# Optimization experiments

Hardware: AMD Instinct MI355X
Metric: run time of the kernel (lower is better)

## Reference

```python
import jax, jax.numpy as jnp
import numpy as np

S, N, B, EMB = 20, 102400, 1024, 64


def setup_inputs() -> dict:
    key = jax.random.key(0)
    ks = jax.random.split(key, 8)
    nodes_abs = jax.random.normal(ks[0], (S, N, 2), jnp.float32) * 5.0
    nodes_norm = jax.random.normal(ks[1], (S, N, 2), jnp.float32)
    shift_value = jax.random.normal(ks[2], (S, N, 2), jnp.float32)
    seq_list = jax.random.uniform(ks[3], (S, N), jnp.float32) - 0.02
    scenes = jnp.arange(B, dtype=jnp.int32)
    pednum = jnp.full((B,), N // B, dtype=jnp.int32)  # peds per scene
    # TSModel stand-in parameters (2 -> EMB -> 2 with GM-history mixing)
    W_in = jax.random.normal(ks[4], (2, EMB), jnp.float32) * 0.5
    W_gm = jax.random.normal(ks[5], (EMB, EMB), jnp.float32) * (1.0 / np.sqrt(EMB))
    b_h = jnp.zeros((EMB,), jnp.float32)
    W_out = jax.random.normal(ks[6], (EMB, 2), jnp.float32) * (1.0 / np.sqrt(EMB))
    b_out = jnp.zeros((2,), jnp.float32)
    return {"nodes_abs": nodes_abs, "nodes_norm": nodes_norm, "shift_value": shift_value,
            "seq_list": seq_list, "scenes": scenes, "pednum": pednum,
            "W_in": W_in, "W_gm": W_gm, "b_h": b_h, "W_out": W_out, "b_out": b_out}


def reference(nodes_abs, nodes_norm, shift_value, seq_list, scenes, pednum,
              W_in, W_gm, b_h, W_out, b_out):
    S_, N_, _ = nodes_abs.shape
    B_ = pednum.shape[0]
    # scene id per pedestrian from cumsum(pednum) -- replaces get_st_ed slices
    scene_ids = jnp.searchsorted(jnp.cumsum(pednum), jnp.arange(N_), side="right")
    presence = seq_list > 0

    def step(carry, xs):
        mask, gm_sum = carry            # mask: [N] peds present in all frames 0..f
        pres_f, abs_f, f = xs
        mask = mask & pres_f            # get_node_index(seq_list[:f+1])
        mf = mask.astype(abs_f.dtype)   # [N]
        # center_alignment_spa: per-scene mean over active peds at frame f
        cnt = jax.ops.segment_sum(mf, scene_ids, num_segments=B_)
        ssum = jax.ops.segment_sum(abs_f * mf[:, None], scene_ids, num_segments=B_)
        center = ssum / jnp.maximum(cnt, 1.0)[:, None]            # [B,2]
        coord = (abs_f - center[scene_ids]) * mf[:, None]         # [N,2]
        # TSModel stand-in: embed centered coord + running GM-history mean
        gm_mean = gm_sum / jnp.maximum(f, 1).astype(gm_sum.dtype)  # mean of GM[:f]
        h = jnp.tanh(coord @ W_in + gm_mean @ W_gm + b_h) * mf[:, None]  # [N,EMB]
        out = (h @ W_out + b_out) * mf[:, None]                    # masked scatter write
        return (mask, gm_sum + h), out

    mask0 = jnp.ones((N_,), dtype=bool)
    gm0 = jnp.zeros((N_, W_gm.shape[0]), nodes_abs.dtype)
    xs = (presence[: S_ - 1], nodes_abs[: S_ - 1], jnp.arange(S_ - 1))
    _, outs = jax.lax.scan(step, (mask0, gm0), xs)                # [S-1,N,2]
    outputs = jnp.concatenate([outs, jnp.zeros((1, N_, 2), outs.dtype)], axis=0)
    return outputs
```

## Files before the change

### kernel.cpp

```cpp
#include <hip/hip_runtime.h>

#define S_DIM 20
#define NSTEP 19
#define EMB   64
#define GSTR  72
#define MAXP  128

typedef __attribute__((ext_vector_type(8))) short bf16x8;
typedef __attribute__((ext_vector_type(4))) float f32x4;

__device__ __forceinline__ uint32_t pk_bf16(float lo, float hi) {
    uint32_t r;
    asm("v_cvt_pk_bf16_f32 %0, %1, %2" : "=v"(r) : "v"(lo), "v"(hi));
    return r;
}
__device__ __forceinline__ short bf16s(float v) { return (short)(pk_bf16(v, v) & 0xffffu); }
__device__ __forceinline__ float unbf16(uint32_t lo16) {
    union { uint32_t u; float f; } c; c.u = lo16 << 16; return c.f;
}

__global__ __launch_bounds__(256, 4) void pfa_kernel(
    const float* __restrict__ nodes_abs,
    const float* __restrict__ seq_list,
    const int*   __restrict__ pednum,
    const float* __restrict__ W_in,
    const float* __restrict__ W_gm,
    const float* __restrict__ b_h,
    const float* __restrict__ W_out,
    const float* __restrict__ b_out,
    float*       __restrict__ out,
    int N, int B)
{
    const int b    = blockIdx.x;
    const int t    = threadIdx.x;
    const int lane = t & 63;
    const int w    = t >> 6;
    const int l15  = lane & 15;
    const int hi   = lane >> 4;

    __shared__ __attribute__((aligned(16))) uint32_t G[8 * 16 * GSTR];
    __shared__ uint32_t masks[MAXP];
    __shared__ float2   cxy[NSTEP];

    int partial = 0;
    for (int i = lane; i < b; i += 64) partial += pednum[i];
    #pragma unroll
    for (int off = 32; off; off >>= 1) partial += __shfl_xor(partial, off, 64);
    const int start = partial;
    const int P = min(pednum[b], MAXP);
    const int q = (P + 7) >> 3;

    {
        uint4* g4 = (uint4*)&G[(w * 2) * 16 * GSTR];
        for (int i = lane; i < 2 * 16 * GSTR / 4; i += 64)
            g4[i] = make_uint4(0u, 0u, 0u, 0u);
    }

    bf16x8 agm[4][2];
    #pragma unroll
    for (int m = 0; m < 4; ++m)
        #pragma unroll
        for (int T = 0; T < 2; ++T)
            #pragma unroll
            for (int e = 0; e < 8; ++e)
                agm[m][T][e] = bf16s(W_gm[(32*T + 8*hi + e) * EMB + 16*m + l15]);

    bf16x8 aaug[4];
    #pragma unroll
    for (int m = 0; m < 4; ++m) {
        bf16x8 a = {0,0,0,0,0,0,0,0};
        if (hi == 0) {
            const int j = 16*m + l15;
            const float w0 = W_in[j], w1 = W_in[EMB + j], bh = b_h[j];
            const short w0h = bf16s(w0); const short w0l = bf16s(w0 - unbf16((uint16_t)w0h));
            const short w1h = bf16s(w1); const short w1l = bf16s(w1 - unbf16((uint16_t)w1h));
            const short bhh = bf16s(bh); const short bhl = bf16s(bh - unbf16((uint16_t)bhh));
            a[0]=w0h; a[1]=w0l; a[2]=w0h; a[3]=w1h; a[4]=w1l; a[5]=w1h; a[6]=bhh; a[7]=bhl;
        }
        aaug[m] = a;
    }

    bf16x8 aout[2];
    #pragma unroll
    for (int T = 0; T < 2; ++T)
        #pragma unroll
        for (int e = 0; e < 8; ++e) {
            const int j = 32*T + 8*hi + e;
            aout[T][e] = (l15 < 2) ? bf16s(W_out[j*2 + l15]) : (short)0;
        }
    const float bo0 = b_out[0], bo1 = b_out[1];

    if (t < P) {
        uint32_t m = 0; bool alive = true;
        #pragma unroll
        for (int f = 0; f < NSTEP; ++f) {
            alive = alive && (seq_list[(size_t)f * N + start + t] > 0.0f);
            m |= (alive ? 1u : 0u) << f;
        }
        masks[t] = m;
    }
    __syncthreads();

    for (int f = w; f < NSTEP; f += 4) {
        float cnt = 0.f, sx = 0.f, sy = 0.f;
        for (int p = lane; p < P; p += 64) {
            const float mf = (float)((masks[p] >> f) & 1u);
            const float2 a = *(const float2*)&nodes_abs[((size_t)f * N + start + p) * 2];
            cnt += mf; sx = fmaf(a.x, mf, sx); sy = fmaf(a.y, mf, sy);
        }
        #pragma unroll
        for (int off = 32; off; off >>= 1) {
            cnt += __shfl_xor(cnt, off, 64);
            sx  += __shfl_xor(sx , off, 64);
            sy  += __shfl_xor(sy , off, 64);
        }
        if (lane == 0) {
            const float ic = __builtin_amdgcn_rcpf(fmaxf(cnt, 1.0f));
            cxy[f] = make_float2(sx * ic, sy * ic);
        }
    }
    __syncthreads();

    bool     vr[2];
    int      gi[2];
    uint32_t mk[2];
    float2   ab[2];
    #pragma unroll
    for (int r = 0; r < 2; ++r) {
        const int pd = 2*q*w + r*q + l15;
        vr[r] = (l15 < q) && (pd < P);
        gi[r] = start + (vr[r] ? pd : 0);
        mk[r] = vr[r] ? masks[pd] : 0u;
        ab[r] = *(const float2*)&nodes_abs[(size_t)gi[r] * 2];
    }

    f32x4 gm[2][4];
    const f32x4 zero4 = {0.f, 0.f, 0.f, 0.f};
    #pragma unroll
    for (int r = 0; r < 2; ++r)
        #pragma unroll
        for (int m = 0; m < 4; ++m) gm[r][m] = zero4;

    const bool h0 = (hi == 0);

    #pragma unroll 1
    for (int f = 0; f < NSTEP; ++f) {
        const float2 c = cxy[f];
        const float invf2 = __builtin_amdgcn_rcpf((float)(f + 1));

        #pragma unroll
        for (int r = 0; r < 2; ++r) {
            uint32_t* const Grow = &G[((w*2 + r) * 16 + l15) * GSTR];
            const float mf  = (float)((mk[r] >> f) & 1u);
            const float cxd = ab[r].x - c.x;
            const float cyd = ab[r].y - c.y;
            ab[r] = *(const float2*)&nodes_abs[((size_t)(f + 1) * N + gi[r]) * 2];

            const uint32_t e0 = pk_bf16(cxd, cxd);
            const float    cxl = cxd - unbf16(e0 & 0xffffu);
            const uint32_t ey = pk_bf16(cyd, cyd);
            const float    cyl = cyd - unbf16(ey & 0xffffu);
            const uint32_t e1 = pk_bf16(cxl, cyd);
            const uint32_t e2 = pk_bf16(cyd, cyl);
            union { uint32_t u[4]; bf16x8 v; } b2u;
            b2u.u[0] = h0 ? e0 : 0u;
            b2u.u[1] = h0 ? e1 : 0u;
            b2u.u[2] = h0 ? e2 : 0u;
            b2u.u[3] = h0 ? 0x3f803f80u : 0u;

            const bf16x8 B0 = *(const bf16x8*)&Grow[ 0 + 4*hi];
            const bf16x8 B1 = *(const bf16x8*)&Grow[16 + 4*hi];

            f32x4 acc[4];
            #pragma unroll
            for (int m = 0; m < 4; ++m) {
                f32x4 cacc = zero4;
                cacc = __builtin_amdgcn_mfma_f32_16x16x32_bf16(aaug[m],   b2u.v, cacc, 0, 0, 0);
                cacc = __builtin_amdgcn_mfma_f32_16x16x32_bf16(agm[m][0], B0,    cacc, 0, 0, 0);
                cacc = __builtin_amdgcn_mfma_f32_16x16x32_bf16(agm[m][1], B1,    cacc, 0, 0, 0);
                acc[m] = cacc;
            }

            const float m2 = -2.0f * mf;
            #pragma unroll
            for (int m = 0; m < 4; ++m) {
                f32x4 h4;
                #pragma unroll
                for (int rr = 0; rr < 4; ++rr) {
                    const float x  = acc[m][rr];
                    const float e  = __expf(2.0f * x);
                    const float tt = __builtin_amdgcn_rcpf(e + 1.0f);
                    h4[rr] = fmaf(tt, m2, mf);
                }
                gm[r][m] += h4;
                const uint32_t p0 = pk_bf16(h4[0], h4[1]);
                const uint32_t p1 = pk_bf16(h4[2], h4[3]);
                *(uint2*)&Grow[32 + 8*m + 2*hi] = make_uint2(p0, p1);
            }

            const bf16x8 H0 = *(const bf16x8*)&Grow[32 + 4*hi];
            const bf16x8 H1 = *(const bf16x8*)&Grow[48 + 4*hi];
            f32x4 oc = zero4;
            oc = __builtin_amdgcn_mfma_f32_16x16x32_bf16(aout[0], H0, oc, 0, 0, 0);
            oc = __builtin_amdgcn_mfma_f32_16x16x32_bf16(aout[1], H1, oc, 0, 0, 0);
            if (h0 && vr[r]) {
                float2 o;
                o.x = (oc[0] + bo0) * mf;
                o.y = (oc[1] + bo1) * mf;
                *(float2*)&out[((size_t)f * N + gi[r]) * 2] = o;
            }

            #pragma unroll
            for (int m = 0; m < 4; ++m) {
                const uint32_t p0 = pk_bf16(gm[r][m][0] * invf2, gm[r][m][1] * invf2);
                const uint32_t p1 = pk_bf16(gm[r][m][2] * invf2, gm[r][m][3] * invf2);
                *(uint2*)&Grow[8*m + 2*hi] = make_uint2(p0, p1);
            }
        }
    }

    if (t < P) {
        const size_t o = ((size_t)(S_DIM - 1) * N + start + t) * 2;
        out[o] = 0.0f; out[o + 1] = 0.0f;
    }
}

extern "C" void kernel_launch(void* const* d_in, const int* in_sizes, int n_in,
                              void* d_out, int out_size, void* d_ws, size_t ws_size,
                              hipStream_t stream) {
    const float* nodes_abs = (const float*)d_in[0];
    const float* seq_list  = (const float*)d_in[3];
    const int*   pednum    = (const int*)  d_in[5];
    const float* W_in      = (const float*)d_in[6];
    const float* W_gm      = (const float*)d_in[7];
    const float* b_h       = (const float*)d_in[8];
    const float* W_out     = (const float*)d_in[9];
    const float* b_out     = (const float*)d_in[10];
    float*       out       = (float*)d_out;

    const int N = in_sizes[3] / S_DIM;
    const int B = in_sizes[5];

    pfa_kernel<<<B, 256, 0, stream>>>(nodes_abs, seq_list, pednum,
                                      W_in, W_gm, b_h, W_out, b_out,
                                      out, N, B);
}
```

Baseline: 105.6 us.

## Split each block's row groups across eight waves instead of four

Blocks now launch 512 threads, so each of 8 waves handles one 16-pedestrian row group instead of each of 4 waves looping over two groups. This shortens each wave's serial per-frame chain and exposes more waves to hide MFMA, transcendental and memory latency. The per-row LDS staging is halved by writing the new hidden state over the same slots that held the history mean once those have been read into registers. In exchange, the launch bound of 512 threads with 4 blocks caps per-thread registers much lower, which could cause spills or lower occupancy, and the two-row interleaving that gave in-wave ILP is lost.

```diff
diff --git a/kernel.cpp b/kernel.cpp
--- a/kernel.cpp
+++ b/kernel.cpp
@@ -3,7 +3,7 @@
 #define S_DIM 20
 #define NSTEP 19
 #define EMB   64
-#define GSTR  72
+#define GSTR  36
 #define MAXP  128
 
 typedef __attribute__((ext_vector_type(8))) short bf16x8;
@@ -19,7 +19,7 @@
     union { uint32_t u; float f; } c; c.u = lo16 << 16; return c.f;
 }
 
-__global__ __launch_bounds__(256, 4) void pfa_kernel(
+__global__ __launch_bounds__(512, 4) void pfa_kernel(
     const float* __restrict__ nodes_abs,
     const float* __restrict__ seq_list,
     const int*   __restrict__ pednum,
@@ -51,8 +51,8 @@
     const int q = (P + 7) >> 3;
 
     {
-        uint4* g4 = (uint4*)&G[(w * 2) * 16 * GSTR];
-        for (int i = lane; i < 2 * 16 * GSTR / 4; i += 64)
+        uint4* g4 = (uint4*)&G[w * 16 * GSTR];
+        for (int i = lane; i < 16 * GSTR / 4; i += 64)
             g4[i] = make_uint4(0u, 0u, 0u, 0u);
     }
 
@@ -101,7 +101,7 @@
     }
     __syncthreads();
 
-    for (int f = w; f < NSTEP; f += 4) {
+    for (int f = w; f < NSTEP; f += 8) {
         float cnt = 0.f, sx = 0.f, sy = 0.f;
         for (int p = lane; p < P; p += 64) {
             const float mf = (float)((masks[p] >> f) & 1u);
@@ -121,101 +121,88 @@
     }
     __syncthreads();
 
-    bool     vr[2];
-    int      gi[2];
-    uint32_t mk[2];
-    float2   ab[2];
-    #pragma unroll
-    for (int r = 0; r < 2; ++r) {
-        const int pd = 2*q*w + r*q + l15;
-        vr[r] = (l15 < q) && (pd < P);
-        gi[r] = start + (vr[r] ? pd : 0);
-        mk[r] = vr[r] ? masks[pd] : 0u;
-        ab[r] = *(const float2*)&nodes_abs[(size_t)gi[r] * 2];
-    }
-
-    f32x4 gm[2][4];
+    const int  pd = w * q + l15;
+    const bool vr = (l15 < q) && (pd < P);
+    const int  gi = start + (vr ? pd : 0);
+    const uint32_t mk = vr ? masks[pd] : 0u;
+    float2 ab = *(const float2*)&nodes_abs[(size_t)gi * 2];
+
+    uint32_t* const Grow = &G[(w * 16 + l15) * GSTR];
+    const bool h0 = (hi == 0);
+
+    f32x4 gm[4];
     const f32x4 zero4 = {0.f, 0.f, 0.f, 0.f};
     #pragma unroll
-    for (int r = 0; r < 2; ++r)
-        #pragma unroll
-        for (int m = 0; m < 4; ++m) gm[r][m] = zero4;
-
-    const bool h0 = (hi == 0);
+    for (int m = 0; m < 4; ++m) gm[m] = zero4;
 
     #pragma unroll 1
     for (int f = 0; f < NSTEP; ++f) {
         const float2 c = cxy[f];
+        const float mf  = (float)((mk >> f) & 1u);
+        const float cxd = ab.x - c.x;
+        const float cyd = ab.y - c.y;
+        ab = *(const float2*)&nodes_abs[((size_t)(f + 1) * N + gi) * 2];
+
+        const uint32_t e0 = pk_bf16(cxd, cxd);
+        const float    cxl = cxd - unbf16(e0 & 0xffffu);
+        const uint32_t ey = pk_bf16(cyd, cyd);
+        const float    cyl = cyd - unbf16(ey & 0xffffu);
+        const uint32_t e1 = pk_bf16(cxl, cyd);
+        const uint32_t e2 = pk_bf16(cyd, cyl);
+        union { uint32_t u[4]; bf16x8 v; } b2u;
+        b2u.u[0] = h0 ? e0 : 0u;
+        b2u.u[1] = h0 ? e1 : 0u;
+        b2u.u[2] = h0 ? e2 : 0u;
+        b2u.u[3] = h0 ? 0x3f803f80u : 0u;
+
+        const bf16x8 B0 = *(const bf16x8*)&Grow[ 0 + 4*hi];
+        const bf16x8 B1 = *(const bf16x8*)&Grow[16 + 4*hi];
+
+        f32x4 acc[4];
+        #pragma unroll
+        for (int m = 0; m < 4; ++m) {
+            f32x4 cacc = zero4;
+            cacc = __builtin_amdgcn_mfma_f32_16x16x32_bf16(aaug[m],   b2u.v, cacc, 0, 0, 0);
+            cacc = __builtin_amdgcn_mfma_f32_16x16x32_bf16(agm[m][0], B0,    cacc, 0, 0, 0);
+            cacc = __builtin_amdgcn_mfma_f32_16x16x32_bf16(agm[m][1], B1,    cacc, 0, 0, 0);
+            acc[m] = cacc;
+        }
+
+        const float m2 = -2.0f * mf;
+        #pragma unroll
+        for (int m = 0; m < 4; ++m) {
+            f32x4 h4;
+            #pragma unroll
+            for (int rr = 0; rr < 4; ++rr) {
+                const float x  = acc[m][rr];
+                const float e  = __expf(2.0f * x);
+                const float tt = __builtin_amdgcn_rcpf(e + 1.0f);
+                h4[rr] = fmaf(tt, m2, mf);
+            }
+            gm[m] += h4;
+            const uint32_t p0 = pk_bf16(h4[0], h4[1]);
+            const uint32_t p1 = pk_bf16(h4[2], h4[3]);
+            *(uint2*)&Grow[8*m + 2*hi] = make_uint2(p0, p1);
+        }
+
+        const bf16x8 H0 = *(const bf16x8*)&Grow[ 0 + 4*hi];
+        const bf16x8 H1 = *(const bf16x8*)&Grow[16 + 4*hi];
+        f32x4 oc = zero4;
+        oc = __builtin_amdgcn_mfma_f32_16x16x32_bf16(aout[0], H0, oc, 0, 0, 0);
+        oc = __builtin_amdgcn_mfma_f32_16x16x32_bf16(aout[1], H1, oc, 0, 0, 0);
+        if (h0 && vr) {
+            float2 o;
+            o.x = (oc[0] + bo0) * mf;
+            o.y = (oc[1] + bo1) * mf;
+            *(float2*)&out[((size_t)f * N + gi) * 2] = o;
+        }
+
         const float invf2 = __builtin_amdgcn_rcpf((float)(f + 1));
-
-        #pragma unroll
-        for (int r = 0; r < 2; ++r) {
-            uint32_t* const Grow = &G[((w*2 + r) * 16 + l15) * GSTR];
-            const float mf  = (float)((mk[r] >> f) & 1u);
-            const float cxd = ab[r].x - c.x;
-            const float cyd = ab[r].y - c.y;
-            ab[r] = *(const float2*)&nodes_abs[((size_t)(f + 1) * N + gi[r]) * 2];
-
-            const uint32_t e0 = pk_bf16(cxd, cxd);
-            const float    cxl = cxd - unbf16(e0 & 0xffffu);
-            const uint32_t ey = pk_bf16(cyd, cyd);
-            const float    cyl = cyd - unbf16(ey & 0xffffu);
-            const uint32_t e1 = pk_bf16(cxl, cyd);
-            const uint32_t e2 = pk_bf16(cyd, cyl);
-            union { uint32_t u[4]; bf16x8 v; } b2u;
-            b2u.u[0] = h0 ? e0 : 0u;
-            b2u.u[1] = h0 ? e1 : 0u;
-            b2u.u[2] = h0 ? e2 : 0u;
-            b2u.u[3] = h0 ? 0x3f803f80u : 0u;
-
-            const bf16x8 B0 = *(const bf16x8*)&Grow[ 0 + 4*hi];
-            const bf16x8 B1 = *(const bf16x8*)&Grow[16 + 4*hi];
-
-            f32x4 acc[4];
-            #pragma unroll
-            for (int m = 0; m < 4; ++m) {
-                f32x4 cacc = zero4;
-                cacc = __builtin_amdgcn_mfma_f32_16x16x32_bf16(aaug[m],   b2u.v, cacc, 0, 0, 0);
-                cacc = __builtin_amdgcn_mfma_f32_16x16x32_bf16(agm[m][0], B0,    cacc, 0, 0, 0);
-                cacc = __builtin_amdgcn_mfma_f32_16x16x32_bf16(agm[m][1], B1,    cacc, 0, 0, 0);
-                acc[m] = cacc;
-            }
-
-            const float m2 = -2.0f * mf;
-            #pragma unroll
-            for (int m = 0; m < 4; ++m) {
-                f32x4 h4;
-                #pragma unroll
-                for (int rr = 0; rr < 4; ++rr) {
-                    const float x  = acc[m][rr];
-                    const float e  = __expf(2.0f * x);
-                    const float tt = __builtin_amdgcn_rcpf(e + 1.0f);
-                    h4[rr] = fmaf(tt, m2, mf);
-                }
-                gm[r][m] += h4;
-                const uint32_t p0 = pk_bf16(h4[0], h4[1]);
-                const uint32_t p1 = pk_bf16(h4[2], h4[3]);
-                *(uint2*)&Grow[32 + 8*m + 2*hi] = make_uint2(p0, p1);
-            }
-
-            const bf16x8 H0 = *(const bf16x8*)&Grow[32 + 4*hi];
-            const bf16x8 H1 = *(const bf16x8*)&Grow[48 + 4*hi];
-            f32x4 oc = zero4;
-            oc = __builtin_amdgcn_mfma_f32_16x16x32_bf16(aout[0], H0, oc, 0, 0, 0);
-            oc = __builtin_amdgcn_mfma_f32_16x16x32_bf16(aout[1], H1, oc, 0, 0, 0);
-            if (h0 && vr[r]) {
-                float2 o;
-                o.x = (oc[0] + bo0) * mf;
-                o.y = (oc[1] + bo1) * mf;
-                *(float2*)&out[((size_t)f * N + gi[r]) * 2] = o;
-            }
-
-            #pragma unroll
-            for (int m = 0; m < 4; ++m) {
-                const uint32_t p0 = pk_bf16(gm[r][m][0] * invf2, gm[r][m][1] * invf2);
-                const uint32_t p1 = pk_bf16(gm[r][m][2] * invf2, gm[r][m][3] * invf2);
-                *(uint2*)&Grow[8*m + 2*hi] = make_uint2(p0, p1);
-            }
+        #pragma unroll
+        for (int m = 0; m < 4; ++m) {
+            const uint32_t p0 = pk_bf16(gm[m][0] * invf2, gm[m][1] * invf2);
+            const uint32_t p1 = pk_bf16(gm[m][2] * invf2, gm[m][3] * invf2);
+            *(uint2*)&Grow[8*m + 2*hi] = make_uint2(p0, p1);
         }
     }
 
@@ -241,7 +228,7 @@
     const int N = in_sizes[3] / S_DIM;
     const int B = in_sizes[5];
 
-    pfa_kernel<<<B, 256, 0, stream>>>(nodes_abs, seq_list, pednum,
+    pfa_kernel<<<B, 512, 0, stream>>>(nodes_abs, seq_list, pednum,
                                       W_in, W_gm, b_h, W_out, b_out,
                                       out, N, B);
 }
```

Result: faster. 87.63 us (-17.0%).

## Replace output MFMA with FMA+shuffle reduction and store raw GM sums

Applied to the files above, without the earlier changes.

Computes the 64->2 output projection with per-lane FMAs against packed bf16 W_out and a cross-lane shuffle reduction, instead of staging h in LDS and running two extra MFMAs. Stores the unscaled GM running sum in LDS and applies 1/f after the MFMA via an FMA, which halves the LDS row stride. It also interleaves both row groups per m so their MFMAs and tanh work can overlap, and lowers the launch-bounds occupancy hint to give the compiler more registers. In exchange it adds per-element FMAs and shuffles, and storing unnormalized sums in bf16 changes rounding behaviour.

```diff
diff --git a/kernel.cpp b/kernel.cpp
--- a/kernel.cpp
+++ b/kernel.cpp
@@ -3,7 +3,7 @@
 #define S_DIM 20
 #define NSTEP 19
 #define EMB   64
-#define GSTR  72
+#define GSTR  36
 #define MAXP  128
 
 typedef __attribute__((ext_vector_type(8))) short bf16x8;
@@ -18,8 +18,11 @@
 __device__ __forceinline__ float unbf16(uint32_t lo16) {
     union { uint32_t u; float f; } c; c.u = lo16 << 16; return c.f;
 }
-
-__global__ __launch_bounds__(256, 4) void pfa_kernel(
+__device__ __forceinline__ float asf(uint32_t u) {
+    union { uint32_t u; float f; } c; c.u = u; return c.f;
+}
+
+__global__ __launch_bounds__(256, 2) void pfa_kernel(
     const float* __restrict__ nodes_abs,
     const float* __restrict__ seq_list,
     const int*   __restrict__ pednum,
@@ -51,9 +54,12 @@
     const int q = (P + 7) >> 3;
 
     {
-        uint4* g4 = (uint4*)&G[(w * 2) * 16 * GSTR];
-        for (int i = lane; i < 2 * 16 * GSTR / 4; i += 64)
-            g4[i] = make_uint4(0u, 0u, 0u, 0u);
+        uint4* g4a = (uint4*)&G[w * 16 * GSTR];
+        uint4* g4b = (uint4*)&G[(w + 4) * 16 * GSTR];
+        for (int i = lane; i < 16 * GSTR / 4; i += 64) {
+            g4a[i] = make_uint4(0u, 0u, 0u, 0u);
+            g4b[i] = make_uint4(0u, 0u, 0u, 0u);
+        }
     }
 
     bf16x8 agm[4][2];
@@ -80,13 +86,13 @@
         aaug[m] = a;
     }
 
-    bf16x8 aout[2];
-    #pragma unroll
-    for (int T = 0; T < 2; ++T)
-        #pragma unroll
-        for (int e = 0; e < 8; ++e) {
-            const int j = 32*T + 8*hi + e;
-            aout[T][e] = (l15 < 2) ? bf16s(W_out[j*2 + l15]) : (short)0;
+    uint32_t wopk[4][4];
+    #pragma unroll
+    for (int m = 0; m < 4; ++m)
+        #pragma unroll
+        for (int rr = 0; rr < 4; ++rr) {
+            const float2 v = *(const float2*)&W_out[(16*m + 4*hi + rr) * 2];
+            wopk[m][rr] = pk_bf16(v.x, v.y);
         }
     const float bo0 = b_out[0], bo1 = b_out[1];
 
@@ -125,14 +131,18 @@
     int      gi[2];
     uint32_t mk[2];
     float2   ab[2];
+    uint32_t* Grow[2];
     #pragma unroll
     for (int r = 0; r < 2; ++r) {
-        const int pd = 2*q*w + r*q + l15;
+        const int rb = w + 4*r;
+        const int pd = rb * q + l15;
         vr[r] = (l15 < q) && (pd < P);
         gi[r] = start + (vr[r] ? pd : 0);
         mk[r] = vr[r] ? masks[pd] : 0u;
         ab[r] = *(const float2*)&nodes_abs[(size_t)gi[r] * 2];
-    }
+        Grow[r] = &G[(rb * 16 + l15) * GSTR];
+    }
+    const bool h0 = (hi == 0);
 
     f32x4 gm[2][4];
     const f32x4 zero4 = {0.f, 0.f, 0.f, 0.f};
@@ -140,81 +150,77 @@
     for (int r = 0; r < 2; ++r)
         #pragma unroll
         for (int m = 0; m < 4; ++m) gm[r][m] = zero4;
-
-    const bool h0 = (hi == 0);
 
     #pragma unroll 1
     for (int f = 0; f < NSTEP; ++f) {
         const float2 c = cxy[f];
-        const float invf2 = __builtin_amdgcn_rcpf((float)(f + 1));
-
+        const float invf = __builtin_amdgcn_rcpf((float)(f ? f : 1));
+
+        float mf[2], m2[2];
+        union { uint32_t u[4]; bf16x8 v; } b2u[2];
         #pragma unroll
         for (int r = 0; r < 2; ++r) {
-            uint32_t* const Grow = &G[((w*2 + r) * 16 + l15) * GSTR];
-            const float mf  = (float)((mk[r] >> f) & 1u);
+            mf[r] = (float)((mk[r] >> f) & 1u);
+            m2[r] = -2.0f * mf[r];
             const float cxd = ab[r].x - c.x;
             const float cyd = ab[r].y - c.y;
             ab[r] = *(const float2*)&nodes_abs[((size_t)(f + 1) * N + gi[r]) * 2];
-
             const uint32_t e0 = pk_bf16(cxd, cxd);
             const float    cxl = cxd - unbf16(e0 & 0xffffu);
             const uint32_t ey = pk_bf16(cyd, cyd);
             const float    cyl = cyd - unbf16(ey & 0xffffu);
             const uint32_t e1 = pk_bf16(cxl, cyd);
             const uint32_t e2 = pk_bf16(cyd, cyl);
-            union { uint32_t u[4]; bf16x8 v; } b2u;
-            b2u.u[0] = h0 ? e0 : 0u;
-            b2u.u[1] = h0 ? e1 : 0u;
-            b2u.u[2] = h0 ? e2 : 0u;
-            b2u.u[3] = h0 ? 0x3f803f80u : 0u;
-
-            const bf16x8 B0 = *(const bf16x8*)&Grow[ 0 + 4*hi];
-            const bf16x8 B1 = *(const bf16x8*)&Grow[16 + 4*hi];
-
-            f32x4 acc[4];
+            b2u[r].u[0] = h0 ? e0 : 0u;
+            b2u[r].u[1] = h0 ? e1 : 0u;
+            b2u[r].u[2] = h0 ? e2 : 0u;
+            b2u[r].u[3] = h0 ? 0x3f803f80u : 0u;
+        }
+
+        bf16x8 B0[2], B1[2];
+        #pragma unroll
+        for (int r = 0; r < 2; ++r) {
+            B0[r] = *(const bf16x8*)&Grow[r][ 0 + 4*hi];
+            B1[r] = *(const bf16x8*)&Grow[r][16 + 4*hi];
+        }
+
+        float o0[2] = {0.0f, 0.0f}, o1[2] = {0.0f, 0.0f};
+        #pragma unroll
+        for (int m = 0; m < 4; ++m) {
             #pragma unroll
-            for (int m = 0; m < 4; ++m) {
-                f32x4 cacc = zero4;
-                cacc = __builtin_amdgcn_mfma_f32_16x16x32_bf16(aaug[m],   b2u.v, cacc, 0, 0, 0);
-                cacc = __builtin_amdgcn_mfma_f32_16x16x32_bf16(agm[m][0], B0,    cacc, 0, 0, 0);
-                cacc = __builtin_amdgcn_mfma_f32_16x16x32_bf16(agm[m][1], B1,    cacc, 0, 0, 0);
-                acc[m] = cacc;
-            }
-
-            const float m2 = -2.0f * mf;
-            #pragma unroll
-            for (int m = 0; m < 4; ++m) {
+            for (int r = 0; r < 2; ++r) {
+                f32x4 ag = zero4;
+                ag = __builtin_amdgcn_mfma_f32_16x16x32_bf16(agm[m][0], B0[r], ag, 0, 0, 0);
+                ag = __builtin_amdgcn_mfma_f32_16x16x32_bf16(agm[m][1], B1[r], ag, 0, 0, 0);
+                f32x4 aa = zero4;
+                aa = __builtin_amdgcn_mfma_f32_16x16x32_bf16(aaug[m], b2u[r].v, aa, 0, 0, 0);
+
                 f32x4 h4;
                 #pragma unroll
                 for (int rr = 0; rr < 4; ++rr) {
-                    const float x  = acc[m][rr];
+                    const float x  = fmaf(ag[rr], invf, aa[rr]);
                     const float e  = __expf(2.0f * x);
                     const float tt = __builtin_amdgcn_rcpf(e + 1.0f);
-                    h4[rr] = fmaf(tt, m2, mf);
+                    h4[rr] = fmaf(tt, m2[r], mf[r]);
+                    o0[r] = fmaf(h4[rr], asf(wopk[m][rr] << 16),         o0[r]);
+                    o1[r] = fmaf(h4[rr], asf(wopk[m][rr] & 0xffff0000u), o1[r]);
                 }
                 gm[r][m] += h4;
-                const uint32_t p0 = pk_bf16(h4[0], h4[1]);
-                const uint32_t p1 = pk_bf16(h4[2], h4[3]);
-                *(uint2*)&Grow[32 + 8*m + 2*hi] = make_uint2(p0, p1);
+                const uint32_t p0 = pk_bf16(gm[r][m][0], gm[r][m][1]);
+                const uint32_t p1 = pk_bf16(gm[r][m][2], gm[r][m][3]);
+                *(uint2*)&Grow[r][8*m + 2*hi] = make_uint2(p0, p1);
             }
-
-            const bf16x8 H0 = *(const bf16x8*)&Grow[32 + 4*hi];
-            const bf16x8 H1 = *(const bf16x8*)&Grow[48 + 4*hi];
-            f32x4 oc = zero4;
-            oc = __builtin_amdgcn_mfma_f32_16x16x32_bf16(aout[0], H0, oc, 0, 0, 0);
-            oc = __builtin_amdgcn_mfma_f32_16x16x32_bf16(aout[1], H1, oc, 0, 0, 0);
+        }
+
+        #pragma unroll
+        for (int r = 0; r < 2; ++r) {
+            o0[r] += __shfl_xor(o0[r], 16, 64);  o0[r] += __shfl_xor(o0[r], 32, 64);
+            o1[r] += __shfl_xor(o1[r], 16, 64);  o1[r] += __shfl_xor(o1[r], 32, 64);
             if (h0 && vr[r]) {
                 float2 o;
-                o.x = (oc[0] + bo0) * mf;
-                o.y = (oc[1] + bo1) * mf;
+                o.x = (o0[r] + bo0) * mf[r];
+                o.y = (o1[r] + bo1) * mf[r];
                 *(float2*)&out[((size_t)f * N + gi[r]) * 2] = o;
-            }
-
-            #pragma unroll
-            for (int m = 0; m < 4; ++m) {
-                const uint32_t p0 = pk_bf16(gm[r][m][0] * invf2, gm[r][m][1] * invf2);
-                const uint32_t p1 = pk_bf16(gm[r][m][2] * invf2, gm[r][m][3] * invf2);
-                *(uint2*)&Grow[8*m + 2*hi] = make_uint2(p0, p1);
             }
         }
     }
```

Result: faster. 95.99 us (-9.1%).
